# Kernel optimization log

Measured on AMD Instinct MI355X. Metric: run time of the kernel, lower is better.

Reference implementation:

```python
import jax, jax.numpy as jnp
import numpy as np

EPS = 1e-5
DN = ('NCHW', 'OIHW', 'NCHW')


def ternarize(w):
    """Ternary Weight Network quantization with straight-through estimator.
    delta = 0.7 * mean|w|; alpha = mean of |w| over kept entries.
    """
    aw = jnp.abs(w)
    delta = 0.7 * aw.mean()
    mask = (aw > delta).astype(w.dtype)
    alpha = (aw * mask).sum() / jnp.maximum(mask.sum(), 1.0)
    q = alpha * jnp.sign(w) * mask
    return w + jax.lax.stop_gradient(q - w)


def bn(y, g, b, m, v):
    scale = (g / jnp.sqrt(v + EPS))[None, :, None, None]
    shift = (b - m * g / jnp.sqrt(v + EPS))[None, :, None, None]
    return y * scale + shift


def relu6(y):
    return jnp.clip(y, 0.0, 6.0)


def conv(x, w, stride=1, padding='VALID'):
    return jax.lax.conv_general_dilated(
        x, w, window_strides=(stride, stride), padding=padding,
        dimension_numbers=DN)


def setup_inputs() -> dict:
    key = jax.random.key(0)
    ks = jax.random.split(key, 16)
    inp, oup, expand = 32, 32, 6
    hidden = inp * expand  # 192
    B, H, W = 16, 112, 112
    d = {}
    d['x'] = jax.random.normal(ks[0], (B, inp, H, W), dtype=jnp.float32)
    # 1x1 expand conv
    d['w1'] = jax.random.normal(ks[1], (hidden, inp, 1, 1), dtype=jnp.float32) * 0.1
    d['g1'] = 1.0 + 0.1 * jax.random.normal(ks[2], (hidden,), dtype=jnp.float32)
    d['b1'] = 0.1 * jax.random.normal(ks[3], (hidden,), dtype=jnp.float32)
    d['m1'] = 0.1 * jax.random.normal(ks[4], (hidden,), dtype=jnp.float32)
    d['v1'] = jax.random.uniform(ks[5], (hidden,), minval=0.5, maxval=1.5, dtype=jnp.float32)
    # 3x3 dense conv (no groups in the source -> dense, not depthwise)
    d['w2'] = jax.random.normal(ks[6], (hidden, hidden, 3, 3), dtype=jnp.float32) * 0.05
    d['g2'] = 1.0 + 0.1 * jax.random.normal(ks[7], (hidden,), dtype=jnp.float32)
    d['b2'] = 0.1 * jax.random.normal(ks[8], (hidden,), dtype=jnp.float32)
    d['m2'] = 0.1 * jax.random.normal(ks[9], (hidden,), dtype=jnp.float32)
    d['v2'] = jax.random.uniform(ks[10], (hidden,), minval=0.5, maxval=1.5, dtype=jnp.float32)
    # 1x1 project conv
    d['w3'] = jax.random.normal(ks[11], (oup, hidden, 1, 1), dtype=jnp.float32) * 0.1
    d['g3'] = 1.0 + 0.1 * jax.random.normal(ks[12], (oup,), dtype=jnp.float32)
    d['b3'] = 0.1 * jax.random.normal(ks[13], (oup,), dtype=jnp.float32)
    d['m3'] = 0.1 * jax.random.normal(ks[14], (oup,), dtype=jnp.float32)
    d['v3'] = jax.random.uniform(ks[15], (oup,), minval=0.5, maxval=1.5, dtype=jnp.float32)
    return d


def reference(x, w1, g1, b1, m1, v1, w2, g2, b2, m2, v2, w3, g3, b3, m3, v3):
    # expand: 1x1 ternary conv -> BN -> ReLU6
    h = relu6(bn(conv(x, ternarize(w1)), g1, b1, m1, v1))
    # 3x3 ternary conv (stride=1, padding=1) -> BN -> ReLU6
    h = relu6(bn(conv(h, ternarize(w2), stride=1, padding=((1, 1), (1, 1))), g2, b2, m2, v2))
    # project: 1x1 ternary conv -> BN (no activation)
    h = bn(conv(h, ternarize(w3)), g3, b3, m3, v3)
    # residual connection (stride==1 and inp==oup)
    return x + h
```

## Files before the change

### kernel.cpp

```cpp
#include <hip/hip_runtime.h>


typedef __bf16 bf16x8 __attribute__((ext_vector_type(8)));
typedef __bf16 bf16x4 __attribute__((ext_vector_type(4)));
typedef float  f32x4  __attribute__((ext_vector_type(4)));

#define EPSBN 1e-5f

__device__ __forceinline__ void glds16(const void* g, void* l) {
  __builtin_amdgcn_global_load_lds(
      (const __attribute__((address_space(1))) void*)g,
      (__attribute__((address_space(3))) void*)l, 16, 0, 0);
}

__device__ __forceinline__ __bf16 tern(float w, float delta) {
  float aw = fabsf(w);
  float q = (aw > delta) ? ((w > 0.0f) ? 1.0f : -1.0f) : 0.0f;
  return (__bf16)q;
}


__global__ void stats_pass1(const float* __restrict__ w1, const float* __restrict__ w2,
                            const float* __restrict__ w3, double* __restrict__ pa) {
  __shared__ double red[256];
  int b = blockIdx.x, tid = threadIdx.x;
  int tix = b >> 5, slice = b & 31;
  const float* w = (tix == 0) ? w1 : (tix == 1) ? w2 : w3;
  int len = (tix == 1) ? 331776 : 6144;
  int per = len >> 5;
  int start = slice * per, end = start + per;
  double s = 0.0;
  for (int i = start + tid; i < end; i += 256) s += (double)fabsf(w[i]);
  red[tid] = s; __syncthreads();
  for (int off = 128; off > 0; off >>= 1) {
    if (tid < off) red[tid] += red[tid + off];
    __syncthreads();
  }
  if (tid == 0) pa[b] = red[0];
}

__global__ void stats_pass2(const float* __restrict__ w1, const float* __restrict__ w2,
                            const float* __restrict__ w3, const double* __restrict__ pa,
                            double* __restrict__ ps2, double* __restrict__ pc2) {
  __shared__ double red[256];
  int b = blockIdx.x, tid = threadIdx.x;
  int tix = b >> 5, slice = b & 31;
  const float* w = (tix == 0) ? w1 : (tix == 1) ? w2 : w3;
  int len = (tix == 1) ? 331776 : 6144;
  double tot = 0.0;
  for (int k = 0; k < 32; ++k) tot += pa[tix * 32 + k];
  float delta = 0.7f * (float)(tot / (double)len);
  int per = len >> 5;
  int start = slice * per, end = start + per;
  double s2 = 0.0, c2 = 0.0;
  for (int i = start + tid; i < end; i += 256) {
    float aw = fabsf(w[i]);
    if (aw > delta) { s2 += (double)aw; c2 += 1.0; }
  }
  red[tid] = s2; __syncthreads();
  for (int off = 128; off > 0; off >>= 1) {
    if (tid < off) red[tid] += red[tid + off];
    __syncthreads();
  }
  if (tid == 0) ps2[b] = red[0];
  __syncthreads();
  red[tid] = c2; __syncthreads();
  for (int off = 128; off > 0; off >>= 1) {
    if (tid < off) red[tid] += red[tid + off];
    __syncthreads();
  }
  if (tid == 0) pc2[b] = red[0];
}

__global__ void stats_pass3(const double* __restrict__ pa, const double* __restrict__ ps2,
                            const double* __restrict__ pc2, float* __restrict__ stats) {
  int tix = blockIdx.x;
  if (threadIdx.x != 0) return;
  double tot = 0.0, s2 = 0.0, c2 = 0.0;
  for (int k = 0; k < 32; ++k) {
    tot += pa[tix * 32 + k];
    s2  += ps2[tix * 32 + k];
    c2  += pc2[tix * 32 + k];
  }
  int len = (tix == 1) ? 331776 : 6144;
  stats[tix * 2]     = 0.7f * (float)(tot / (double)len);
  stats[tix * 2 + 1] = (float)(s2 / fmax(c2, 1.0));
}

__global__ void pack_kernel(
    const float* __restrict__ w1, const float* __restrict__ w2, const float* __restrict__ w3,
    const float* __restrict__ g1, const float* __restrict__ b1, const float* __restrict__ m1, const float* __restrict__ v1,
    const float* __restrict__ g2, const float* __restrict__ b2, const float* __restrict__ m2, const float* __restrict__ v2,
    const float* __restrict__ g3, const float* __restrict__ b3, const float* __restrict__ m3, const float* __restrict__ v3,
    const float* __restrict__ stats,
    __bf16* __restrict__ w1p, __bf16* __restrict__ w2p, __bf16* __restrict__ w3p,
    float* __restrict__ sc1, float* __restrict__ sh1,
    float* __restrict__ sc2, float* __restrict__ sh2,
    float* __restrict__ sc3, float* __restrict__ sh3) {
  int idx = blockIdx.x * 256 + threadIdx.x;
  if (idx < 331776) {
    float delta2 = stats[2];
    int c = idx / 6144, rem = idx - c * 6144;
    int co = rem >> 5, r5 = rem & 31;
    int cp = r5 >> 3, lo = r5 & 7;
    int tap = c / 6, cb = c - tap * 6;
    int ci = ((cp ^ ((co >> 2) & 3)) << 3) | lo;
    int cifull = cb * 32 + ci;
    w2p[idx] = tern(w2[(co * 192 + cifull) * 9 + tap], delta2);
    return;
  }
  idx -= 331776;
  if (idx < 6144) {
    int co = idx >> 5, c = (idx >> 3) & 3, lo = idx & 7;
    int ci = ((c ^ ((co >> 2) & 3)) << 3) | lo;
    w1p[idx] = tern(w1[co * 32 + ci], stats[0]);
    return;
  }
  idx -= 6144;
  if (idx < 6144) {
    int kc = idx >> 11, rem = idx & 2047;
    int co = rem >> 6, c = (rem >> 3) & 7, lo = rem & 7;
    int ci = ((c ^ (co & 7)) << 3) | lo;
    w3p[idx] = tern(w3[co * 192 + kc * 64 + ci], stats[4]);
    return;
  }
  idx -= 6144;
  if (idx < 192) {
    float rs = rsqrtf(v1[idx] + EPSBN);
    sc1[idx] = g1[idx] * rs * stats[1];
    sh1[idx] = b1[idx] - m1[idx] * g1[idx] * rs;
    return;
  }
  idx -= 192;
  if (idx < 192) {
    float rs = rsqrtf(v2[idx] + EPSBN);
    sc2[idx] = g2[idx] * rs * stats[3];
    sh2[idx] = b2[idx] - m2[idx] * g2[idx] * rs;
    return;
  }
  idx -= 192;
  if (idx < 32) {
    float rs = rsqrtf(v3[idx] + EPSBN);
    sc3[idx] = g3[idx] * rs * stats[5];
    sh3[idx] = b3[idx] - m3[idx] * g3[idx] * rs;
  }
}

__global__ __launch_bounds__(256)
void conv1_kernel(const float* __restrict__ x, const __bf16* __restrict__ w1p,
                  const float* __restrict__ scale1, const float* __restrict__ shift1,
                  __bf16* __restrict__ h1p) {
  __shared__ __bf16 smA[112 * 32];
  __shared__ __bf16 smB[192 * 32];
  int tid = threadIdx.x, lane = tid & 63, wave = tid >> 6;
  int h = blockIdx.x, n = blockIdx.y;

  for (int t = wave; t < 12; t += 4)
    glds16((const char*)w1p + t * 1024 + lane * 16, (char*)smB + t * 1024);

  const float* xrow = x + (long)n * 401408 + h * 112;
  for (int i = 0; i < 14; ++i) {
    int f = i * 256 + tid;
    int ci = f / 112, w = f - ci * 112;
    int col = ((ci >> 3) ^ ((w >> 2) & 3));
    smA[w * 32 + (col << 3) + (ci & 7)] = (__bf16)xrow[ci * 12544 + w];
  }
  __syncthreads();

  int mrow = lane & 15, quad = lane >> 4;
  int col16 = (quad ^ ((mrow >> 2) & 3)) * 16;
  int c0 = wave * 48;

  bf16x8 aw[3], bv[7];
#pragma unroll
  for (int ic = 0; ic < 3; ++ic)
    aw[ic] = *(const bf16x8*)((const char*)smB + (c0 + ic * 16 + mrow) * 64 + col16);
#pragma unroll
  for (int jp = 0; jp < 7; ++jp)
    bv[jp] = *(const bf16x8*)((const char*)smA + (jp * 16 + mrow) * 64 + col16);

  f32x4 acc[7][3];
#pragma unroll
  for (int jp = 0; jp < 7; ++jp)
#pragma unroll
    for (int ic = 0; ic < 3; ++ic) acc[jp][ic] = (f32x4)0.0f;

#pragma unroll
  for (int jp = 0; jp < 7; ++jp)
#pragma unroll
    for (int ic = 0; ic < 3; ++ic)
      acc[jp][ic] = __builtin_amdgcn_mfma_f32_16x16x32_bf16(aw[ic], bv[jp], acc[jp][ic], 0, 0, 0);

  __bf16* obase = h1p + ((long)(n * 114 + h + 1) * 114 + 1) * 192;
#pragma unroll
  for (int ic = 0; ic < 3; ++ic) {
    int co0 = c0 + ic * 16 + quad * 4;
    float4 sc = *(const float4*)(scale1 + co0);
    float4 sh = *(const float4*)(shift1 + co0);
#pragma unroll
    for (int jp = 0; jp < 7; ++jp) {
      int w = jp * 16 + mrow;
      bf16x4 o;
      o[0] = (__bf16)fminf(fmaxf(acc[jp][ic][0] * sc.x + sh.x, 0.0f), 6.0f);
      o[1] = (__bf16)fminf(fmaxf(acc[jp][ic][1] * sc.y + sh.y, 0.0f), 6.0f);
      o[2] = (__bf16)fminf(fmaxf(acc[jp][ic][2] * sc.z + sh.z, 0.0f), 6.0f);
      o[3] = (__bf16)fminf(fmaxf(acc[jp][ic][3] * sc.w + sh.w, 0.0f), 6.0f);
      *(bf16x4*)(obase + w * 192 + co0) = o;
    }
  }

  float4 z = make_float4(0.f, 0.f, 0.f, 0.f);
  if (tid < 48) {
    int px = (tid < 24) ? 0 : 113;
    int c8 = (tid < 24) ? tid : tid - 24;
    *(float4*)((char*)h1p + ((long)((n * 114 + h + 1) * 114 + px) * 384) + c8 * 16) = z;
  }
  if (h == 0) {
    for (int c = tid; c < 2736; c += 256)
      *(float4*)((char*)h1p + (long)(n * 114) * 114 * 384 + c * 16) = z;
  }
  if (h == 111) {
    for (int c = tid; c < 2736; c += 256)
      *(float4*)((char*)h1p + (long)(n * 114 + 113) * 114 * 384 + c * 16) = z;
  }
}


#define STAGE_W(TAP, CB, B) do {                                              \
  _Pragma("unroll")                                                           \
  for (int it_ = 0; it_ < 3; ++it_) {                                         \
    int t_ = wave + it_ * 4;                                                  \
    glds16(w2b + (long)((TAP) * 6 + (CB)) * 12288 + t_ * 1024 + lane * 16,    \
           (char*)smB + (B) * 12288 + t_ * 1024);                             \
  }                                                                           \
} while (0)

#define STAGE_A(CB) do {                                                      \
  _Pragma("unroll")                                                           \
  for (int it_ = 0; it_ < 8; ++it_)                                           \
    if (aoff[it_] >= 0)                                                       \
      glds16(h1b + aoff[it_] + (CB) * 64, (char*)smA + (wave + it_ * 4) * 1024); \
} while (0)

__global__ __launch_bounds__(256, 2)
void conv2_kernel(const __bf16* __restrict__ h1p, const __bf16* __restrict__ w2p,
                  const float* __restrict__ scale2, const float* __restrict__ shift2,
                  __bf16* __restrict__ h2) {
  __shared__ __bf16 smA[456 * 32];
  __shared__ __bf16 smB[4 * 192 * 32];
  int tid = threadIdx.x, lane = tid & 63, wave = tid >> 6;
  int bh = blockIdx.x, n = blockIdx.y;
  int h0 = bh * 2;

  int aoff[8];
#pragma unroll
  for (int it = 0; it < 8; ++it) {
    int t = wave + it * 4;
    int s = t * 64 + lane;
    if (s < 1824) {
      int q = s >> 2, c = s & 3;
      int q_log = c ^ ((q >> 2) & 3);
      int prow = q / 114, pcol = q - prow * 114;
      aoff[it] = ((n * 114 + h0 + prow) * 114 + pcol) * 384 + q_log * 16;
    } else {
      aoff[it] = -1;
    }
  }

  int pg = wave >> 1, cg = wave & 1;
  int mrow = lane & 15, quad = lane >> 4;
  int col16 = (quad ^ ((mrow >> 2) & 3)) * 16;
  const char* h1b = (const char*)h1p;
  const char* w2b = (const char*)w2p;

  f32x4 acc[7][6];
#pragma unroll
  for (int jp = 0; jp < 7; ++jp)
#pragma unroll
    for (int ic = 0; ic < 6; ++ic) acc[jp][ic] = (f32x4)0.0f;

  STAGE_A(0);
  STAGE_W(0, 0, 0);
  STAGE_W(1, 0, 1);

  for (int cb = 0; cb < 6; ++cb) {
#pragma unroll
    for (int tap = 0; tap < 9; ++tap) {
      if (tap <= 6) {
        STAGE_W(tap + 2, cb, (tap + 2) & 3);
        asm volatile("s_waitcnt vmcnt(6)" ::: "memory");
      } else if (tap == 7) {
        asm volatile("s_waitcnt vmcnt(3)" ::: "memory");
      } else {
        asm volatile("s_waitcnt vmcnt(0)" ::: "memory");
      }
      __builtin_amdgcn_s_barrier();
      __builtin_amdgcn_sched_barrier(0);

      const char* bbuf = (const char*)smB + (tap & 3) * 12288;
      bf16x8 aw[6];
#pragma unroll
      for (int ic = 0; ic < 6; ++ic)
        aw[ic] = *(const bf16x8*)(bbuf + (cg * 96 + ic * 16 + mrow) * 64 + col16);

      int dy = tap / 3, dx = tap - dy * 3;
      int base = (pg + dy) * 114 + dx;
      __builtin_amdgcn_s_setprio(1);
#pragma unroll
      for (int jp = 0; jp < 7; ++jp) {
        int row = base + jp * 16 + mrow;
        bf16x8 av = *(const bf16x8*)((const char*)smA + row * 64 +
                                     ((quad ^ ((row >> 2) & 3)) * 16));
#pragma unroll
        for (int ic = 0; ic < 6; ++ic)
          acc[jp][ic] = __builtin_amdgcn_mfma_f32_16x16x32_bf16(aw[ic], av, acc[jp][ic], 0, 0, 0);
      }
      __builtin_amdgcn_s_setprio(0);
    }

    if (cb < 5) {
      asm volatile("s_waitcnt lgkmcnt(0)" ::: "memory");
      __builtin_amdgcn_sched_barrier(0);
      __builtin_amdgcn_s_barrier();
      STAGE_A(cb + 1);
      STAGE_W(0, cb + 1, 0);
      STAGE_W(1, cb + 1, 1);
    }
  }

  int h = h0 + pg;
  __bf16* orow = h2 + (long)((n * 112 + h) * 112) * 192;
#pragma unroll
  for (int ic = 0; ic < 6; ++ic) {
    int co0 = cg * 96 + ic * 16 + quad * 4;
    float4 sc = *(const float4*)(scale2 + co0);
    float4 sh = *(const float4*)(shift2 + co0);
#pragma unroll
    for (int jp = 0; jp < 7; ++jp) {
      int w = jp * 16 + mrow;
      bf16x4 o;
      o[0] = (__bf16)fminf(fmaxf(acc[jp][ic][0] * sc.x + sh.x, 0.0f), 6.0f);
      o[1] = (__bf16)fminf(fmaxf(acc[jp][ic][1] * sc.y + sh.y, 0.0f), 6.0f);
      o[2] = (__bf16)fminf(fmaxf(acc[jp][ic][2] * sc.z + sh.z, 0.0f), 6.0f);
      o[3] = (__bf16)fminf(fmaxf(acc[jp][ic][3] * sc.w + sh.w, 0.0f), 6.0f);
      *(bf16x4*)(orow + w * 192 + co0) = o;
    }
  }
}

__global__ __launch_bounds__(128)
void conv3_kernel(const __bf16* __restrict__ h2, const __bf16* __restrict__ w3p,
                  const float* __restrict__ scale3, const float* __restrict__ shift3,
                  const float* __restrict__ x, float* __restrict__ out) {
  __shared__ __bf16 smA[112 * 64];
  __shared__ __bf16 smB[32 * 64];
  int tid = threadIdx.x, lane = tid & 63, wv = tid >> 6;
  int h = blockIdx.x, n = blockIdx.y;
  int mrow = lane & 15, quad = lane >> 4;
  int swz7 = mrow & 7;

  const char* h2b = (const char*)h2 + (long)((n * 112 + h) * 112) * 384;
  f32x4 acc[7];
#pragma unroll
  for (int i = 0; i < 7; ++i) acc[i] = (f32x4)0.0f;

  for (int kc = 0; kc < 3; ++kc) {
    for (int t = wv; t < 18; t += 2) {
      if (t < 14) {
        int slot = t * 64 + lane;
        int w = slot >> 3, s = slot & 7;
        glds16(h2b + w * 384 + kc * 128 + (s ^ (w & 7)) * 16, (char*)smA + t * 1024);
      } else {
        glds16((const char*)w3p + kc * 4096 + (t - 14) * 1024 + lane * 16,
               (char*)smB + (t - 14) * 1024);
      }
    }
    __syncthreads();
    bf16x8 a[7][2], b[2];
#pragma unroll
    for (int ks = 0; ks < 2; ++ks) {
      int col = ((ks * 4 + quad) ^ swz7) * 16;
      b[ks] = *(const bf16x8*)((const char*)smB + (wv * 16 + mrow) * 128 + col);
#pragma unroll
      for (int i = 0; i < 7; ++i)
        a[i][ks] = *(const bf16x8*)((const char*)smA + (i * 16 + mrow) * 128 + col);
    }
    __syncthreads();
#pragma unroll
    for (int ks = 0; ks < 2; ++ks)
#pragma unroll
      for (int i = 0; i < 7; ++i)
        acc[i] = __builtin_amdgcn_mfma_f32_16x16x32_bf16(a[i][ks], b[ks], acc[i], 0, 0, 0);
  }

  int co = wv * 16 + mrow;
  float sc = scale3[co], sh = shift3[co];
  long obase = ((long)(n * 32 + co) * 112 + h) * 112;
  const float* xb = x + obase;
  float* ob = out + obase;
#pragma unroll
  for (int i = 0; i < 7; ++i) {
    int w0 = i * 16 + quad * 4;
    float4 xv = *(const float4*)(xb + w0);
    float4 o;
    o.x = acc[i][0] * sc + sh + xv.x;
    o.y = acc[i][1] * sc + sh + xv.y;
    o.z = acc[i][2] * sc + sh + xv.z;
    o.w = acc[i][3] * sc + sh + xv.w;
    *(float4*)(ob + w0) = o;
  }
}

extern "C" void kernel_launch(void* const* d_in, const int* in_sizes, int n_in,
                              void* d_out, int out_size, void* d_ws, size_t ws_size,
                              hipStream_t stream) {
  const float* x  = (const float*)d_in[0];
  const float* w1 = (const float*)d_in[1];
  const float* g1 = (const float*)d_in[2];
  const float* b1 = (const float*)d_in[3];
  const float* m1 = (const float*)d_in[4];
  const float* v1 = (const float*)d_in[5];
  const float* w2 = (const float*)d_in[6];
  const float* g2 = (const float*)d_in[7];
  const float* b2 = (const float*)d_in[8];
  const float* m2 = (const float*)d_in[9];
  const float* v2 = (const float*)d_in[10];
  const float* w3 = (const float*)d_in[11];
  const float* g3 = (const float*)d_in[12];
  const float* b3 = (const float*)d_in[13];
  const float* m3 = (const float*)d_in[14];
  const float* v3 = (const float*)d_in[15];
  float* out = (float*)d_out;

  char* ws = (char*)d_ws;
  float*  stats = (float*)ws;
  double* pa    = (double*)(ws + 256);
  double* ps2   = (double*)(ws + 1024);
  double* pc2   = (double*)(ws + 1792);
  float* sc1 = (float*)(ws + 2560);
  float* sh1 = (float*)(ws + 3328);
  float* sc2 = (float*)(ws + 4096);
  float* sh2 = (float*)(ws + 4864);
  float* sc3 = (float*)(ws + 5632);
  float* sh3 = (float*)(ws + 5760);
  __bf16* w1p = (__bf16*)(ws + 8192);
  __bf16* w3p = (__bf16*)(ws + 20480);
  __bf16* w2p = (__bf16*)(ws + 32768);
  __bf16* h1p = (__bf16*)(ws + (1 << 20));
  __bf16* h2  = (__bf16*)(ws + (1 << 20) + 79847424);

  hipLaunchKernelGGL(stats_pass1, dim3(96), dim3(256), 0, stream, w1, w2, w3, pa);
  hipLaunchKernelGGL(stats_pass2, dim3(96), dim3(256), 0, stream, w1, w2, w3, pa, ps2, pc2);
  hipLaunchKernelGGL(stats_pass3, dim3(3), dim3(64), 0, stream, pa, ps2, pc2, stats);
  hipLaunchKernelGGL(pack_kernel, dim3(1346), dim3(256), 0, stream, w1, w2, w3,
                     g1, b1, m1, v1, g2, b2, m2, v2, g3, b3, m3, v3, stats,
                     w1p, w2p, w3p, sc1, sh1, sc2, sh2, sc3, sh3);
  hipLaunchKernelGGL(conv1_kernel, dim3(112, 16), dim3(256), 0, stream, x, w1p, sc1, sh1, h1p);
  hipLaunchKernelGGL(conv2_kernel, dim3(56, 16), dim3(256), 0, stream, h1p, w2p, sc2, sh2, h2);
  hipLaunchKernelGGL(conv3_kernel, dim3(112, 16), dim3(128), 0, stream, h2, w3p, sc3, sh3, x, out);
}
```

Before: 295.6 us.

## Fuse 1x1 project conv and residual into 3x3 conv kernel epilogue

New measurement: 267.1 us. 1.11x faster.

```diff
diff --git a/kernel.cpp b/kernel.cpp
--- a/kernel.cpp
+++ b/kernel.cpp
@@ -231,7 +231,7 @@
   for (int it_ = 0; it_ < 3; ++it_) {                                         \
     int t_ = wave + it_ * 4;                                                  \
     glds16(w2b + (long)((TAP) * 6 + (CB)) * 12288 + t_ * 1024 + lane * 16,    \
-           (char*)smB + (B) * 12288 + t_ * 1024);                             \
+           smBb + (B) * 12288 + t_ * 1024);                                   \
   }                                                                           \
 } while (0)
 
@@ -239,15 +239,20 @@
   _Pragma("unroll")                                                           \
   for (int it_ = 0; it_ < 8; ++it_)                                           \
     if (aoff[it_] >= 0)                                                       \
-      glds16(h1b + aoff[it_] + (CB) * 64, (char*)smA + (wave + it_ * 4) * 1024); \
+      glds16(h1b + aoff[it_] + (CB) * 64, smAb + (wave + it_ * 4) * 1024);    \
 } while (0)
 
 __global__ __launch_bounds__(256, 2)
 void conv2_kernel(const __bf16* __restrict__ h1p, const __bf16* __restrict__ w2p,
                   const float* __restrict__ scale2, const float* __restrict__ shift2,
-                  __bf16* __restrict__ h2) {
-  __shared__ __bf16 smA[456 * 32];
-  __shared__ __bf16 smB[4 * 192 * 32];
+                  const __bf16* __restrict__ w3p,
+                  const float* __restrict__ scale3, const float* __restrict__ shift3,
+                  const float* __restrict__ x, float* __restrict__ out) {
+  __shared__ __align__(16) char smem[78336];
+  char* smAb = smem;
+  char* smBb = smem + 29184;
+  char* Pb   = smem;
+  char* w3l  = smem + 43008;
   int tid = threadIdx.x, lane = tid & 63, wave = tid >> 6;
   int bh = blockIdx.x, n = blockIdx.y;
   int h0 = bh * 2;
@@ -297,7 +302,7 @@
       __builtin_amdgcn_s_barrier();
       __builtin_amdgcn_sched_barrier(0);
 
-      const char* bbuf = (const char*)smB + (tap & 3) * 12288;
+      const char* bbuf = smBb + (tap & 3) * 12288;
       bf16x8 aw[6];
 #pragma unroll
       for (int ic = 0; ic < 6; ++ic)
@@ -309,7 +314,7 @@
 #pragma unroll
       for (int jp = 0; jp < 7; ++jp) {
         int row = base + jp * 16 + mrow;
-        bf16x8 av = *(const bf16x8*)((const char*)smA + row * 64 +
+        bf16x8 av = *(const bf16x8*)(smAb + row * 64 +
                                      ((quad ^ ((row >> 2) & 3)) * 16));
 #pragma unroll
         for (int ic = 0; ic < 6; ++ic)
@@ -328,86 +333,93 @@
     }
   }
 
-  int h = h0 + pg;
-  __bf16* orow = h2 + (long)((n * 112 + h) * 112) * 192;
-#pragma unroll
-  for (int ic = 0; ic < 6; ++ic) {
-    int co0 = cg * 96 + ic * 16 + quad * 4;
-    float4 sc = *(const float4*)(scale2 + co0);
-    float4 sh = *(const float4*)(shift2 + co0);
-#pragma unroll
-    for (int jp = 0; jp < 7; ++jp) {
-      int w = jp * 16 + mrow;
-      bf16x4 o;
-      o[0] = (__bf16)fminf(fmaxf(acc[jp][ic][0] * sc.x + sh.x, 0.0f), 6.0f);
-      o[1] = (__bf16)fminf(fmaxf(acc[jp][ic][1] * sc.y + sh.y, 0.0f), 6.0f);
-      o[2] = (__bf16)fminf(fmaxf(acc[jp][ic][2] * sc.z + sh.z, 0.0f), 6.0f);
-      o[3] = (__bf16)fminf(fmaxf(acc[jp][ic][3] * sc.w + sh.w, 0.0f), 6.0f);
-      *(bf16x4*)(orow + w * 192 + co0) = o;
-    }
-  }
-}
-
-__global__ __launch_bounds__(128)
-void conv3_kernel(const __bf16* __restrict__ h2, const __bf16* __restrict__ w3p,
-                  const float* __restrict__ scale3, const float* __restrict__ shift3,
-                  const float* __restrict__ x, float* __restrict__ out) {
-  __shared__ __bf16 smA[112 * 64];
-  __shared__ __bf16 smB[32 * 64];
-  int tid = threadIdx.x, lane = tid & 63, wv = tid >> 6;
-  int h = blockIdx.x, n = blockIdx.y;
-  int mrow = lane & 15, quad = lane >> 4;
-  int swz7 = mrow & 7;
-
-  const char* h2b = (const char*)h2 + (long)((n * 112 + h) * 112) * 384;
-  f32x4 acc[7];
-#pragma unroll
-  for (int i = 0; i < 7; ++i) acc[i] = (f32x4)0.0f;
-
-  for (int kc = 0; kc < 3; ++kc) {
-    for (int t = wv; t < 18; t += 2) {
-      if (t < 14) {
-        int slot = t * 64 + lane;
-        int w = slot >> 3, s = slot & 7;
-        glds16(h2b + w * 384 + kc * 128 + (s ^ (w & 7)) * 16, (char*)smA + t * 1024);
-      } else {
-        glds16((const char*)w3p + kc * 4096 + (t - 14) * 1024 + lane * 16,
-               (char*)smB + (t - 14) * 1024);
+  asm volatile("s_waitcnt lgkmcnt(0)" ::: "memory");
+  __builtin_amdgcn_s_barrier();
+  __builtin_amdgcn_sched_barrier(0);
+
+#pragma unroll
+  for (int it = 0; it < 3; ++it) {
+    int t = wave + it * 4;
+    glds16((const char*)w3p + t * 1024 + lane * 16, w3l + t * 1024);
+  }
+
+  int cohalf = wave & 1;
+  int co3 = cohalf * 16 + mrow;
+  float sc3v = scale3[co3], sh3v = shift3[co3];
+  int fbase = (wave >> 1) * 4;
+
+#pragma unroll
+  for (int rg = 0; rg < 2; ++rg) {
+    if (pg == rg) {
+#pragma unroll
+      for (int ic = 0; ic < 6; ++ic) {
+        int co0 = cg * 96 + ic * 16 + quad * 4;
+        float4 sc = *(const float4*)(scale2 + co0);
+        float4 sh = *(const float4*)(shift2 + co0);
+        int kc = co0 >> 6, c6 = co0 & 63;
+        int chunk = c6 >> 3, off = c6 & 7;
+#pragma unroll
+        for (int jp = 0; jp < 7; ++jp) {
+          int px = jp * 16 + mrow;
+          bf16x4 o;
+          o[0] = (__bf16)fminf(fmaxf(acc[jp][ic][0] * sc.x + sh.x, 0.0f), 6.0f);
+          o[1] = (__bf16)fminf(fmaxf(acc[jp][ic][1] * sc.y + sh.y, 0.0f), 6.0f);
+          o[2] = (__bf16)fminf(fmaxf(acc[jp][ic][2] * sc.z + sh.z, 0.0f), 6.0f);
+          o[3] = (__bf16)fminf(fmaxf(acc[jp][ic][3] * sc.w + sh.w, 0.0f), 6.0f);
+          *(bf16x4*)(Pb + px * 384 + kc * 128 + ((chunk ^ (px & 7)) * 16) + off * 2) = o;
+        }
       }
     }
-    __syncthreads();
-    bf16x8 a[7][2], b[2];
-#pragma unroll
-    for (int ks = 0; ks < 2; ++ks) {
-      int col = ((ks * 4 + quad) ^ swz7) * 16;
-      b[ks] = *(const bf16x8*)((const char*)smB + (wv * 16 + mrow) * 128 + col);
-#pragma unroll
-      for (int i = 0; i < 7; ++i)
-        a[i][ks] = *(const bf16x8*)((const char*)smA + (i * 16 + mrow) * 128 + col);
-    }
-    __syncthreads();
-#pragma unroll
-    for (int ks = 0; ks < 2; ++ks)
-#pragma unroll
-      for (int i = 0; i < 7; ++i)
-        acc[i] = __builtin_amdgcn_mfma_f32_16x16x32_bf16(a[i][ks], b[ks], acc[i], 0, 0, 0);
-  }
-
-  int co = wv * 16 + mrow;
-  float sc = scale3[co], sh = shift3[co];
-  long obase = ((long)(n * 32 + co) * 112 + h) * 112;
-  const float* xb = x + obase;
-  float* ob = out + obase;
-#pragma unroll
-  for (int i = 0; i < 7; ++i) {
-    int w0 = i * 16 + quad * 4;
-    float4 xv = *(const float4*)(xb + w0);
-    float4 o;
-    o.x = acc[i][0] * sc + sh + xv.x;
-    o.y = acc[i][1] * sc + sh + xv.y;
-    o.z = acc[i][2] * sc + sh + xv.z;
-    o.w = acc[i][3] * sc + sh + xv.w;
-    *(float4*)(ob + w0) = o;
+    if (rg == 0)
+      asm volatile("s_waitcnt vmcnt(0) lgkmcnt(0)" ::: "memory");
+    else
+      asm volatile("s_waitcnt lgkmcnt(0)" ::: "memory");
+    __builtin_amdgcn_s_barrier();
+    __builtin_amdgcn_sched_barrier(0);
+
+    f32x4 acc3[4];
+#pragma unroll
+    for (int f = 0; f < 4; ++f) acc3[f] = (f32x4)0.0f;
+    int swz = mrow & 7;
+#pragma unroll
+    for (int kc = 0; kc < 3; ++kc) {
+      bf16x8 b0 = *(const bf16x8*)(w3l + kc * 4096 + (cohalf * 16 + mrow) * 128 +
+                                   ((quad ^ swz) * 16));
+      bf16x8 b1 = *(const bf16x8*)(w3l + kc * 4096 + (cohalf * 16 + mrow) * 128 +
+                                   (((4 + quad) ^ swz) * 16));
+#pragma unroll
+      for (int f = 0; f < 4; ++f) {
+        if (fbase + f < 7) {
+          int pr = (fbase + f) * 16 + mrow;
+          bf16x8 a0 = *(const bf16x8*)(Pb + pr * 384 + kc * 128 + ((quad ^ swz) * 16));
+          bf16x8 a1 = *(const bf16x8*)(Pb + pr * 384 + kc * 128 + (((4 + quad) ^ swz) * 16));
+          acc3[f] = __builtin_amdgcn_mfma_f32_16x16x32_bf16(a0, b0, acc3[f], 0, 0, 0);
+          acc3[f] = __builtin_amdgcn_mfma_f32_16x16x32_bf16(a1, b1, acc3[f], 0, 0, 0);
+        }
+      }
+    }
+    int h = h0 + rg;
+    long obase = ((long)(n * 32 + co3) * 112 + h) * 112;
+    const float* xb = x + obase;
+    float* ob = out + obase;
+#pragma unroll
+    for (int f = 0; f < 4; ++f) {
+      if (fbase + f < 7) {
+        int w0 = (fbase + f) * 16 + quad * 4;
+        float4 xv = *(const float4*)(xb + w0);
+        float4 o;
+        o.x = acc3[f][0] * sc3v + sh3v + xv.x;
+        o.y = acc3[f][1] * sc3v + sh3v + xv.y;
+        o.z = acc3[f][2] * sc3v + sh3v + xv.z;
+        o.w = acc3[f][3] * sc3v + sh3v + xv.w;
+        *(float4*)(ob + w0) = o;
+      }
+    }
+    if (rg == 0) {
+      asm volatile("s_waitcnt lgkmcnt(0)" ::: "memory");
+      __builtin_amdgcn_s_barrier();
+      __builtin_amdgcn_sched_barrier(0);
+    }
   }
 }
 
@@ -447,7 +459,6 @@
   __bf16* w3p = (__bf16*)(ws + 20480);
   __bf16* w2p = (__bf16*)(ws + 32768);
   __bf16* h1p = (__bf16*)(ws + (1 << 20));
-  __bf16* h2  = (__bf16*)(ws + (1 << 20) + 79847424);
 
   hipLaunchKernelGGL(stats_pass1, dim3(96), dim3(256), 0, stream, w1, w2, w3, pa);
   hipLaunchKernelGGL(stats_pass2, dim3(96), dim3(256), 0, stream, w1, w2, w3, pa, ps2, pc2);
@@ -456,6 +467,6 @@
                      g1, b1, m1, v1, g2, b2, m2, v2, g3, b3, m3, v3, stats,
                      w1p, w2p, w3p, sc1, sh1, sc2, sh2, sc3, sh3);
   hipLaunchKernelGGL(conv1_kernel, dim3(112, 16), dim3(256), 0, stream, x, w1p, sc1, sh1, h1p);
-  hipLaunchKernelGGL(conv2_kernel, dim3(56, 16), dim3(256), 0, stream, h1p, w2p, sc2, sh2, h2);
-  hipLaunchKernelGGL(conv3_kernel, dim3(112, 16), dim3(128), 0, stream, h2, w3p, sc3, sh3, x, out);
-}
+  hipLaunchKernelGGL(conv2_kernel, dim3(56, 16), dim3(256), 0, stream, h1p, w2p, sc2, sh2,
+                     w3p, sc3, sh3, x, out);
+}
```
